# Performance work log

Measured on AMD Instinct MI355X. Metric: run time of the kernel, lower is better.

Reference implementation:

```python
import jax, jax.numpy as jnp
import numpy as np

B, QN, KVN = 4, 512, 512
QD, KD, H, VD = 512, 512, 256, 256


def setup_inputs() -> dict:
    key = jax.random.key(0)
    ks = jax.random.split(key, 6)
    q = jax.random.normal(ks[0], (B, QN, QD), dtype=jnp.float32)
    k = jax.random.normal(ks[1], (B, KVN, KD), dtype=jnp.float32)
    v = jax.random.normal(ks[2], (B, KVN, VD), dtype=jnp.float32)
    # Linear weights (torch nn.Linear stores [out, in]; bias=False)
    Wq = jax.random.normal(ks[3], (H, QD), dtype=jnp.float32) / np.sqrt(QD)
    Wk = jax.random.normal(ks[4], (H, KD), dtype=jnp.float32) / np.sqrt(KD)
    wv = jax.random.normal(ks[5], (H,), dtype=jnp.float32) / np.sqrt(H)
    return {"q": q, "k": k, "v": v, "Wq": Wq, "Wk": Wk, "wv": wv}


def reference(q, k, v, Wq, Wk, wv):
    # Project queries and keys to hidden dim H
    qh = jnp.einsum("bqd,hd->bqh", q, Wq)  # [B, QN, H]
    kh = jnp.einsum("bkd,hd->bkh", k, Wk)  # [B, KVN, H]
    # Broadcast add + tanh: [B, QN, KVN, H]
    energy = jnp.tanh(qh[:, :, None, :] + kh[:, None, :, :])
    # Score projection to scalar per (q, kv) pair
    scores = jnp.einsum("bqkh,h->bqk", energy, wv)  # [B, QN, KVN]
    attention = jax.nn.softmax(scores, axis=-1)
    # Dropout omitted (inference mode)
    output = jnp.einsum("bqk,bkv->bqv", attention, v)  # [B, QN, VD]
    return (output, attention)
```

## Files before the change

### kernel.cpp

```cpp
#include <hip/hip_runtime.h>

#define B_ 4
#define QN 512
#define KVN 512
#define QD_ 512
#define H_ 256
#define VD_ 256
#define TOTR 2048

typedef __attribute__((ext_vector_type(8))) short bf16x8;
typedef __attribute__((ext_vector_type(4))) float f32x4;
typedef __attribute__((ext_vector_type(2))) float f32x2;
typedef __attribute__((ext_vector_type(4))) unsigned short u16x4;
typedef unsigned short u16;

__device__ __forceinline__ float rcp_(float x) { return __builtin_amdgcn_rcpf(x); }
__device__ __forceinline__ float ex2_(float x) { return __builtin_amdgcn_exp2f(x); }

__device__ __forceinline__ u16 bf16_rne(float x) {
    unsigned u = __float_as_uint(x);
    unsigned r = u + 0x7FFFu + ((u >> 16) & 1u);
    return (u16)(r >> 16);
}
__device__ __forceinline__ void split2(float x, u16& h, u16& l) {
    h = bf16_rne(x);
    float hf = __uint_as_float((unsigned)h << 16);
    l = bf16_rne(x - hf);
}
__device__ __forceinline__ void split4(float4 a, u16x4& h, u16x4& l) {
    u16 hh, ll;
    split2(a.x, hh, ll); h[0] = hh; l[0] = ll;
    split2(a.y, hh, ll); h[1] = hh; l[1] = ll;
    split2(a.z, hh, ll); h[2] = hh; l[2] = ll;
    split2(a.w, hh, ll); h[3] = hh; l[3] = ll;
}

__global__ __launch_bounds__(256) void prep(const float* __restrict__ q,
                                            const float* __restrict__ k,
                                            const float* __restrict__ Wq,
                                            const float* __restrict__ Wk,
                                            const float* __restrict__ v,
                                            u16* __restrict__ q_hi, u16* __restrict__ q_lo,
                                            u16* __restrict__ k_hi, u16* __restrict__ k_lo,
                                            u16* __restrict__ w_hi, u16* __restrict__ w_lo,
                                            u16* __restrict__ vt_hi, u16* __restrict__ vt_lo) {
    __shared__ float ts[64][65];
    const int tid = threadIdx.x;
    if (blockIdx.x < 2304) {
        const int NQ = 2048 * 512 / 4, NW = 256 * 512 / 4;
        int idx = blockIdx.x * 256 + tid;
        const float* src; u16 *dh, *dl; int off;
        if (idx < NQ)               { src = q;  dh = q_hi; dl = q_lo; off = idx; }
        else if (idx < 2 * NQ)      { src = k;  dh = k_hi; dl = k_lo; off = idx - NQ; }
        else if (idx < 2 * NQ + NW) { src = Wq; dh = w_hi; dl = w_lo; off = idx - 2 * NQ; }
        else { src = Wk; dh = w_hi + 256 * 512; dl = w_lo + 256 * 512; off = idx - 2 * NQ - NW; }
        float4 v4 = ((const float4*)src)[off];
        u16x4 h, l;
        split4(v4, h, l);
        *(u16x4*)(dh + off * 4) = h;
        *(u16x4*)(dl + off * 4) = l;
    } else {
        int bid = blockIdx.x - 2304;
        int j0 = (bid & 7) * 64, n0 = ((bid >> 3) & 3) * 64, b = bid >> 5;
#pragma unroll
        for (int t = 0; t < 4; ++t) {
            int idx = t * 256 + tid;
            int j = idx >> 4, nq = idx & 15;
            float4 v4 = *(const float4*)(v + ((size_t)b * KVN + j0 + j) * VD_ + n0 + nq * 4);
            *(float4*)&ts[j][nq * 4] = v4;
        }
        __syncthreads();
#pragma unroll
        for (int t = 0; t < 4; ++t) {
            int idx = t * 256 + tid;
            int jq = idx & 15, n = idx >> 4;
            u16x4 h, l;
            u16 hh, ll;
#pragma unroll
            for (int e = 0; e < 4; ++e) {
                split2(ts[jq * 4 + e][n], hh, ll);
                h[e] = hh; l[e] = ll;
            }
            size_t off = ((size_t)b * VD_ + n0 + n) * KVN + j0 + jq * 4;
            *(u16x4*)(vt_hi + off) = h;
            *(u16x4*)(vt_lo + off) = l;
        }
    }
}

__global__ __launch_bounds__(256) void proj_mfma(const u16* __restrict__ q_hi, const u16* __restrict__ q_lo,
                                                 const u16* __restrict__ k_hi, const u16* __restrict__ k_lo,
                                                 const u16* __restrict__ w_hi, const u16* __restrict__ w_lo,
                                                 float* __restrict__ eqT, float* __restrict__ ek) {
    const int z = blockIdx.z;
    const u16* __restrict__ Ah_g = z ? k_hi : q_hi;
    const u16* __restrict__ Al_g = z ? k_lo : q_lo;
    const u16* __restrict__ Bh_g = w_hi + (size_t)z * H_ * QD_;
    const u16* __restrict__ Bl_g = w_lo + (size_t)z * H_ * QD_;
    __shared__ u16 Ash[4][32][8], Asl[4][32][8], Bsh[4][32][8], Bsl[4][32][8];
    const int tid = threadIdx.x;
    const int wave = tid >> 6, lane = tid & 63;
    const int fl = lane & 15, kg = lane >> 4;
    const int r0 = blockIdx.y * 32, c0 = blockIdx.x * 32;
    const int ar = 16 * (wave & 1), bc = 16 * (wave >> 1);
    const int frow = (tid & 127) >> 2, fkq = tid & 3, fsel = tid >> 7;
    f32x4 acc = {};
    for (int k0 = 0; k0 < QD_; k0 += 32) {
        __syncthreads();
        {
            const u16* as = (fsel ? Al_g : Ah_g) + (size_t)(r0 + frow) * QD_ + k0 + fkq * 8;
            u16* ad = fsel ? &Asl[fkq][frow][0] : &Ash[fkq][frow][0];
            *(uint4*)ad = *(const uint4*)as;
            const u16* bs = (fsel ? Bl_g : Bh_g) + (size_t)(c0 + frow) * QD_ + k0 + fkq * 8;
            u16* bd = fsel ? &Bsl[fkq][frow][0] : &Bsh[fkq][frow][0];
            *(uint4*)bd = *(const uint4*)bs;
        }
        __syncthreads();
        bf16x8 a_h = *(const bf16x8*)&Ash[kg][ar + fl][0];
        bf16x8 a_l = *(const bf16x8*)&Asl[kg][ar + fl][0];
        bf16x8 b_h = *(const bf16x8*)&Bsh[kg][bc + fl][0];
        bf16x8 b_l = *(const bf16x8*)&Bsl[kg][bc + fl][0];
        acc = __builtin_amdgcn_mfma_f32_16x16x32_bf16(a_h, b_h, acc, 0, 0, 0);
        acc = __builtin_amdgcn_mfma_f32_16x16x32_bf16(a_h, b_l, acc, 0, 0, 0);
        acc = __builtin_amdgcn_mfma_f32_16x16x32_bf16(a_l, b_h, acc, 0, 0, 0);
    }
    const float cs = 2.8853900817779268f;
    const int rg = kg * 4;
    if (z == 0) {
        float4 o = {ex2_(acc[0] * cs), ex2_(acc[1] * cs), ex2_(acc[2] * cs), ex2_(acc[3] * cs)};
        *(float4*)(eqT + (size_t)(c0 + bc + fl) * TOTR + r0 + ar + rg) = o;
    } else {
#pragma unroll
        for (int r = 0; r < 4; ++r)
            ek[(size_t)(r0 + ar + rg + r) * H_ + c0 + bc + fl] = ex2_(acc[r] * cs);
    }
}

__device__ __forceinline__ f32x2 col4(const f32x2* qp, float4 kc, float4 w4, f32x2 acc) {
    const f32x2 one = {1.0f, 1.0f};
    f32x2 d0 = __builtin_elementwise_fma(qp[0], (f32x2){kc.x, kc.x}, one);
    f32x2 d1 = __builtin_elementwise_fma(qp[1], (f32x2){kc.y, kc.y}, one);
    f32x2 d2 = __builtin_elementwise_fma(qp[2], (f32x2){kc.z, kc.z}, one);
    f32x2 d3 = __builtin_elementwise_fma(qp[3], (f32x2){kc.w, kc.w}, one);
    f32x2 ab = d0 * d1, cd = d2 * d3;
    f32x2 n1 = __builtin_elementwise_fma((f32x2){w4.y, w4.y}, d0, (f32x2){w4.x, w4.x} * d1);
    f32x2 n2 = __builtin_elementwise_fma((f32x2){w4.w, w4.w}, d2, (f32x2){w4.z, w4.z} * d3);
    f32x2 num = __builtin_elementwise_fma(n2, ab, n1 * cd);
    f32x2 den = ab * cd;
    f32x2 r = {rcp_(den.x), rcp_(den.y)};
    return __builtin_elementwise_fma(num, r, acc);
}

__global__ __launch_bounds__(256, 8) void scores_v5(const float* __restrict__ eqT,
                                                    const float* __restrict__ ek,
                                                    const float* __restrict__ wv,
                                                    float* __restrict__ scpart) {
    __shared__ f32x2 qs[32][32];
    __shared__ float ks[64][36];
    const int bz = blockIdx.z;
    const int b = bz >> 3, hs = bz & 7;
    const int h0 = hs * 32;
    const int i0 = blockIdx.y * 64, j0 = blockIdx.x * 64;
    const int tid = threadIdx.x;
    const int qq = tid & 15, kq = tid >> 4;
#pragma unroll
    for (int t = 0; t < 4; ++t) {
        int idx = t * 256 + tid;
        int hq = idx >> 5, pr = idx & 31;
        qs[hq][pr] = *(const f32x2*)(eqT + (size_t)(h0 + hq) * TOTR + b * QN + i0 + 2 * pr);
    }
#pragma unroll
    for (int t = 0; t < 2; ++t) {
        int idx = t * 256 + tid;
        int row = idx >> 3, c4 = idx & 7;
        *(float4*)&ks[row][c4 * 4] =
            *(const float4*)(ek + (size_t)(b * KVN + j0 + row) * H_ + h0 + c4 * 4);
    }
    __syncthreads();
    f32x2 acc[2][4] = {};
#pragma unroll
    for (int hh = 0; hh < 32; hh += 4) {
        float4 w4 = *(const float4*)(wv + h0 + hh);
        f32x2 qp0[4], qp1[4];
#pragma unroll
        for (int e = 0; e < 4; ++e) {
            float4 Q = *(const float4*)&qs[hh + e][2 * qq];
            qp0[e].x = Q.x; qp0[e].y = Q.y;
            qp1[e].x = Q.z; qp1[e].y = Q.w;
        }
#pragma unroll
        for (int r = 0; r < 4; ++r) {
            float4 K = *(const float4*)&ks[4 * kq + r][hh];
            acc[0][r] = col4(qp0, K, w4, acc[0][r]);
            acc[1][r] = col4(qp1, K, w4, acc[1][r]);
        }
    }
    float* base = scpart + (size_t)hs * TOTR * KVN +
                  (size_t)(b * QN + i0 + 4 * qq) * KVN + j0 + 4 * kq;
    float4 o0 = {-2.f * acc[0][0].x, -2.f * acc[0][1].x, -2.f * acc[0][2].x, -2.f * acc[0][3].x};
    float4 o1 = {-2.f * acc[0][0].y, -2.f * acc[0][1].y, -2.f * acc[0][2].y, -2.f * acc[0][3].y};
    float4 o2 = {-2.f * acc[1][0].x, -2.f * acc[1][1].x, -2.f * acc[1][2].x, -2.f * acc[1][3].x};
    float4 o3 = {-2.f * acc[1][0].y, -2.f * acc[1][1].y, -2.f * acc[1][2].y, -2.f * acc[1][3].y};
    *(float4*)(base) = o0;
    *(float4*)(base + KVN) = o1;
    *(float4*)(base + 2 * KVN) = o2;
    *(float4*)(base + 3 * KVN) = o3;
}

__global__ __launch_bounds__(256) void softmax2(const float* __restrict__ scpart,
                                                float* __restrict__ attn,
                                                u16* __restrict__ at_hi,
                                                u16* __restrict__ at_lo) {
    const size_t PS = (size_t)TOTR * KVN;
    int row = blockIdx.x;
    int tid = threadIdx.x;
    const float* p = scpart + (size_t)row * KVN;
    float x0 = 0.f, x1 = 0.f;
#pragma unroll
    for (int hsplit = 0; hsplit < 8; ++hsplit) {
        x0 += p[hsplit * PS + tid];
        x1 += p[hsplit * PS + tid + 256];
    }
    float e0 = __expf(x0), e1 = __expf(x1);
    float s = e0 + e1;
#pragma unroll
    for (int d = 1; d < 64; d <<= 1) s += __shfl_xor(s, d);
    __shared__ float reds[4];
    int wave = tid >> 6, lane = tid & 63;
    if (lane == 0) reds[wave] = s;
    __syncthreads();
    s = reds[0] + reds[1] + reds[2] + reds[3];
    float inv = rcp_(s);
    float r0v = e0 * inv, r1v = e1 * inv;
    float* o = attn + (size_t)row * KVN;
    o[tid] = r0v;
    o[tid + 256] = r1v;
    u16 h, l;
    size_t base = (size_t)row * KVN;
    split2(r0v, h, l);
    at_hi[base + tid] = h; at_lo[base + tid] = l;
    split2(r1v, h, l);
    at_hi[base + tid + 256] = h; at_lo[base + tid + 256] = l;
}

__global__ __launch_bounds__(256) void out_mfma(const u16* __restrict__ vt_hi, const u16* __restrict__ vt_lo,
                                                const u16* __restrict__ at_hi, const u16* __restrict__ at_lo,
                                                float* __restrict__ out) {
    const int b = blockIdx.z;
    const u16* __restrict__ Ah_g = vt_hi + (size_t)b * VD_ * KVN;
    const u16* __restrict__ Al_g = vt_lo + (size_t)b * VD_ * KVN;
    const u16* __restrict__ Bh_g = at_hi + (size_t)b * QN * KVN;
    const u16* __restrict__ Bl_g = at_lo + (size_t)b * QN * KVN;
    float* __restrict__ outb = out + (size_t)b * QN * VD_;
    __shared__ u16 Ash[4][32][8], Asl[4][32][8], Bsh[4][32][8], Bsl[4][32][8];
    const int tid = threadIdx.x;
    const int wave = tid >> 6, lane = tid & 63;
    const int fl = lane & 15, kg = lane >> 4;
    const int r0 = blockIdx.y * 32;
    const int c0 = blockIdx.x * 32;
    const int ar = 16 * (wave & 1), bc = 16 * (wave >> 1);
    const int frow = (tid & 127) >> 2, fkq = tid & 3, fsel = tid >> 7;
    f32x4 acc = {};
    for (int k0 = 0; k0 < KVN; k0 += 32) {
        __syncthreads();
        {
            const u16* as = (fsel ? Al_g : Ah_g) + (size_t)(r0 + frow) * KVN + k0 + fkq * 8;
            u16* ad = fsel ? &Asl[fkq][frow][0] : &Ash[fkq][frow][0];
            *(uint4*)ad = *(const uint4*)as;
            const u16* bs = (fsel ? Bl_g : Bh_g) + (size_t)(c0 + frow) * KVN + k0 + fkq * 8;
            u16* bd = fsel ? &Bsl[fkq][frow][0] : &Bsh[fkq][frow][0];
            *(uint4*)bd = *(const uint4*)bs;
        }
        __syncthreads();
        bf16x8 a_h = *(const bf16x8*)&Ash[kg][ar + fl][0];
        bf16x8 a_l = *(const bf16x8*)&Asl[kg][ar + fl][0];
        bf16x8 b_h = *(const bf16x8*)&Bsh[kg][bc + fl][0];
        bf16x8 b_l = *(const bf16x8*)&Bsl[kg][bc + fl][0];
        acc = __builtin_amdgcn_mfma_f32_16x16x32_bf16(a_h, b_h, acc, 0, 0, 0);
        acc = __builtin_amdgcn_mfma_f32_16x16x32_bf16(a_h, b_l, acc, 0, 0, 0);
        acc = __builtin_amdgcn_mfma_f32_16x16x32_bf16(a_l, b_h, acc, 0, 0, 0);
    }
    const int rg = kg * 4;
    float4 o = {acc[0], acc[1], acc[2], acc[3]};
    *(float4*)(outb + (size_t)(c0 + bc + fl) * VD_ + r0 + ar + rg) = o;
}

extern "C" void kernel_launch(void* const* d_in, const int* in_sizes, int n_in,
                              void* d_out, int out_size, void* d_ws, size_t ws_size,
                              hipStream_t stream) {
    const float* q  = (const float*)d_in[0];
    const float* k  = (const float*)d_in[1];
    const float* v  = (const float*)d_in[2];
    const float* Wq = (const float*)d_in[3];
    const float* Wk = (const float*)d_in[4];
    const float* wv = (const float*)d_in[5];
    float* out  = (float*)d_out;
    float* attn = out + (size_t)B_ * QN * VD_;

    float* eqT = (float*)d_ws;
    float* ek  = eqT + H_ * TOTR;
    u16* q_hi = (u16*)(ek + TOTR * H_);
    u16* q_lo = q_hi + 2048 * 512;
    u16* k_hi = q_lo + 2048 * 512;
    u16* k_lo = k_hi + 2048 * 512;
    u16* w_hi = k_lo + 2048 * 512;
    u16* w_lo = w_hi + 512 * 512;
    u16* vt_hi = w_lo + 512 * 512;
    u16* vt_lo = vt_hi + (size_t)B_ * VD_ * KVN;
    float* scpart = (float*)(vt_lo + (size_t)B_ * VD_ * KVN);
    u16* at_hi = q_hi;
    u16* at_lo = q_lo;

    prep<<<2432, 256, 0, stream>>>(q, k, Wq, Wk, v, q_hi, q_lo, k_hi, k_lo,
                                   w_hi, w_lo, vt_hi, vt_lo);
    proj_mfma<<<dim3(H_ / 32, 2048 / 32, 2), 256, 0, stream>>>(q_hi, q_lo, k_hi, k_lo,
                                                               w_hi, w_lo, eqT, ek);
    scores_v5<<<dim3(KVN / 64, QN / 64, B_ * 8), 256, 0, stream>>>(eqT, ek, wv, scpart);
    softmax2<<<TOTR, 256, 0, stream>>>(scpart, attn, at_hi, at_lo);
    out_mfma<<<dim3(QN / 32, VD_ / 32, B_), 256, 0, stream>>>(vt_hi, vt_lo, at_hi, at_lo, out);
}
```

Measured before the change: 70.38 us.

## Restructure scores kernel to keep key energies in registers and broadcast queries

Swaps which projection is stored transposed: query energies are now row-major and key energies are transposed. The scores kernel drops shared memory. Each thread keeps 32 key-energy values for one kv column in registers and loops over 32 query rows, reading wave-uniform query vectors straight from global memory. This removes LDS staging and syncs, but each thread now does scalar per-pair work instead of a 2x4 register tile, and global loads depend on cache broadcast.

```diff
diff --git a/kernel.cpp b/kernel.cpp
--- a/kernel.cpp
+++ b/kernel.cpp
@@ -10,7 +10,6 @@
 
 typedef __attribute__((ext_vector_type(8))) short bf16x8;
 typedef __attribute__((ext_vector_type(4))) float f32x4;
-typedef __attribute__((ext_vector_type(2))) float f32x2;
 typedef __attribute__((ext_vector_type(4))) unsigned short u16x4;
 typedef unsigned short u16;
 
@@ -91,7 +90,7 @@
 __global__ __launch_bounds__(256) void proj_mfma(const u16* __restrict__ q_hi, const u16* __restrict__ q_lo,
                                                  const u16* __restrict__ k_hi, const u16* __restrict__ k_lo,
                                                  const u16* __restrict__ w_hi, const u16* __restrict__ w_lo,
-                                                 float* __restrict__ eqT, float* __restrict__ ek) {
+                                                 float* __restrict__ eq, float* __restrict__ ekT) {
     const int z = blockIdx.z;
     const u16* __restrict__ Ah_g = z ? k_hi : q_hi;
     const u16* __restrict__ Al_g = z ? k_lo : q_lo;
@@ -126,85 +125,60 @@
     }
     const float cs = 2.8853900817779268f;
     const int rg = kg * 4;
-    if (z == 0) {
+    if (z == 1) {
         float4 o = {ex2_(acc[0] * cs), ex2_(acc[1] * cs), ex2_(acc[2] * cs), ex2_(acc[3] * cs)};
-        *(float4*)(eqT + (size_t)(c0 + bc + fl) * TOTR + r0 + ar + rg) = o;
+        *(float4*)(ekT + (size_t)(c0 + bc + fl) * TOTR + r0 + ar + rg) = o;
     } else {
 #pragma unroll
         for (int r = 0; r < 4; ++r)
-            ek[(size_t)(r0 + ar + rg + r) * H_ + c0 + bc + fl] = ex2_(acc[r] * cs);
-    }
-}
-
-__device__ __forceinline__ f32x2 col4(const f32x2* qp, float4 kc, float4 w4, f32x2 acc) {
-    const f32x2 one = {1.0f, 1.0f};
-    f32x2 d0 = __builtin_elementwise_fma(qp[0], (f32x2){kc.x, kc.x}, one);
-    f32x2 d1 = __builtin_elementwise_fma(qp[1], (f32x2){kc.y, kc.y}, one);
-    f32x2 d2 = __builtin_elementwise_fma(qp[2], (f32x2){kc.z, kc.z}, one);
-    f32x2 d3 = __builtin_elementwise_fma(qp[3], (f32x2){kc.w, kc.w}, one);
-    f32x2 ab = d0 * d1, cd = d2 * d3;
-    f32x2 n1 = __builtin_elementwise_fma((f32x2){w4.y, w4.y}, d0, (f32x2){w4.x, w4.x} * d1);
-    f32x2 n2 = __builtin_elementwise_fma((f32x2){w4.w, w4.w}, d2, (f32x2){w4.z, w4.z} * d3);
-    f32x2 num = __builtin_elementwise_fma(n2, ab, n1 * cd);
-    f32x2 den = ab * cd;
-    f32x2 r = {rcp_(den.x), rcp_(den.y)};
-    return __builtin_elementwise_fma(num, r, acc);
-}
-
-__global__ __launch_bounds__(256, 8) void scores_v5(const float* __restrict__ eqT,
-                                                    const float* __restrict__ ek,
+            eq[(size_t)(r0 + ar + rg + r) * H_ + c0 + bc + fl] = ex2_(acc[r] * cs);
+    }
+}
+
+__global__ __launch_bounds__(256, 8) void scores_v6(const float* __restrict__ eq,
+                                                    const float* __restrict__ ekT,
                                                     const float* __restrict__ wv,
                                                     float* __restrict__ scpart) {
-    __shared__ f32x2 qs[32][32];
-    __shared__ float ks[64][36];
-    const int bz = blockIdx.z;
-    const int b = bz >> 3, hs = bz & 7;
+    const int tid = threadIdx.x;
+    const int wid = tid >> 6, lane = tid & 63;
+    const int hs = blockIdx.z;
     const int h0 = hs * 32;
-    const int i0 = blockIdx.y * 64, j0 = blockIdx.x * 64;
-    const int tid = threadIdx.x;
-    const int qq = tid & 15, kq = tid >> 4;
-#pragma unroll
-    for (int t = 0; t < 4; ++t) {
-        int idx = t * 256 + tid;
-        int hq = idx >> 5, pr = idx & 31;
-        qs[hq][pr] = *(const f32x2*)(eqT + (size_t)(h0 + hq) * TOTR + b * QN + i0 + 2 * pr);
-    }
-#pragma unroll
-    for (int t = 0; t < 2; ++t) {
-        int idx = t * 256 + tid;
-        int row = idx >> 3, c4 = idx & 7;
-        *(float4*)&ks[row][c4 * 4] =
-            *(const float4*)(ek + (size_t)(b * KVN + j0 + row) * H_ + h0 + c4 * 4);
-    }
-    __syncthreads();
-    f32x2 acc[2][4] = {};
-#pragma unroll
-    for (int hh = 0; hh < 32; hh += 4) {
-        float4 w4 = *(const float4*)(wv + h0 + hh);
-        f32x2 qp0[4], qp1[4];
-#pragma unroll
-        for (int e = 0; e < 4; ++e) {
-            float4 Q = *(const float4*)&qs[hh + e][2 * qq];
-            qp0[e].x = Q.x; qp0[e].y = Q.y;
-            qp1[e].x = Q.z; qp1[e].y = Q.w;
-        }
-#pragma unroll
-        for (int r = 0; r < 4; ++r) {
-            float4 K = *(const float4*)&ks[4 * kq + r][hh];
-            acc[0][r] = col4(qp0, K, w4, acc[0][r]);
-            acc[1][r] = col4(qp1, K, w4, acc[1][r]);
-        }
-    }
-    float* base = scpart + (size_t)hs * TOTR * KVN +
-                  (size_t)(b * QN + i0 + 4 * qq) * KVN + j0 + 4 * kq;
-    float4 o0 = {-2.f * acc[0][0].x, -2.f * acc[0][1].x, -2.f * acc[0][2].x, -2.f * acc[0][3].x};
-    float4 o1 = {-2.f * acc[0][0].y, -2.f * acc[0][1].y, -2.f * acc[0][2].y, -2.f * acc[0][3].y};
-    float4 o2 = {-2.f * acc[1][0].x, -2.f * acc[1][1].x, -2.f * acc[1][2].x, -2.f * acc[1][3].x};
-    float4 o3 = {-2.f * acc[1][0].y, -2.f * acc[1][1].y, -2.f * acc[1][2].y, -2.f * acc[1][3].y};
-    *(float4*)(base) = o0;
-    *(float4*)(base + KVN) = o1;
-    *(float4*)(base + 2 * KVN) = o2;
-    *(float4*)(base + 3 * KVN) = o3;
+    const int row0 = blockIdx.y * 32;
+    const int b = row0 >> 9;
+    const int jloc = blockIdx.x * 256 + wid * 64 + lane;
+    const int colg = b * KVN + jloc;
+
+    float ekr[32];
+#pragma unroll
+    for (int hh = 0; hh < 32; ++hh)
+        ekr[hh] = ekT[(size_t)(h0 + hh) * TOTR + colg];
+
+    float4 wr[8];
+#pragma unroll
+    for (int g = 0; g < 8; ++g) wr[g] = *(const float4*)(wv + h0 + g * 4);
+
+    const float* __restrict__ eqrow = eq + (size_t)row0 * H_ + h0;
+    float* __restrict__ outp = scpart + (size_t)hs * TOTR * KVN + (size_t)row0 * KVN + jloc;
+
+#pragma unroll 4
+    for (int qq = 0; qq < 32; ++qq) {
+        const float* ep = eqrow + (size_t)qq * H_;
+        float s = 0.f;
+#pragma unroll
+        for (int g = 0; g < 8; ++g) {
+            float4 e = *(const float4*)(ep + 4 * g);
+            float a  = __builtin_fmaf(ekr[4 * g + 0], e.x, 1.0f);
+            float bb = __builtin_fmaf(ekr[4 * g + 1], e.y, 1.0f);
+            float cc = __builtin_fmaf(ekr[4 * g + 2], e.z, 1.0f);
+            float dd = __builtin_fmaf(ekr[4 * g + 3], e.w, 1.0f);
+            float ab = a * bb, cd = cc * dd;
+            float n1 = __builtin_fmaf(wr[g].y, a, wr[g].x * bb);
+            float n2 = __builtin_fmaf(wr[g].w, cc, wr[g].z * dd);
+            float num = __builtin_fmaf(n2, ab, n1 * cd);
+            s = __builtin_fmaf(num, rcp_(ab * cd), s);
+        }
+        outp[(size_t)qq * KVN] = -2.0f * s;
+    }
 }
 
 __global__ __launch_bounds__(256) void softmax2(const float* __restrict__ scpart,
@@ -297,9 +271,9 @@
     float* out  = (float*)d_out;
     float* attn = out + (size_t)B_ * QN * VD_;
 
-    float* eqT = (float*)d_ws;
-    float* ek  = eqT + H_ * TOTR;
-    u16* q_hi = (u16*)(ek + TOTR * H_);
+    float* eq  = (float*)d_ws;
+    float* ekT = eq + (size_t)TOTR * H_;
+    u16* q_hi = (u16*)(ekT + (size_t)H_ * TOTR);
     u16* q_lo = q_hi + 2048 * 512;
     u16* k_hi = q_lo + 2048 * 512;
     u16* k_lo = k_hi + 2048 * 512;
@@ -314,8 +288,8 @@
     prep<<<2432, 256, 0, stream>>>(q, k, Wq, Wk, v, q_hi, q_lo, k_hi, k_lo,
                                    w_hi, w_lo, vt_hi, vt_lo);
     proj_mfma<<<dim3(H_ / 32, 2048 / 32, 2), 256, 0, stream>>>(q_hi, q_lo, k_hi, k_lo,
-                                                               w_hi, w_lo, eqT, ek);
-    scores_v5<<<dim3(KVN / 64, QN / 64, B_ * 8), 256, 0, stream>>>(eqT, ek, wv, scpart);
+                                                               w_hi, w_lo, eq, ekT);
+    scores_v6<<<dim3(2, TOTR / 32, 8), 256, 0, stream>>>(eq, ekT, wv, scpart);
     softmax2<<<TOTR, 256, 0, stream>>>(scpart, attn, at_hi, at_lo);
     out_mfma<<<dim3(QN / 32, VD_ / 32, B_), 256, 0, stream>>>(vt_hi, vt_lo, at_hi, at_lo, out);
 }
```

New measurement: 83.17 us. +18.2%, slower.
